# Kernel tuning notes

Hardware: AMD Instinct MI355X
Metric: run time of the kernel (lower is better)

The kernel has to match this reference:

```python
import jax, jax.numpy as jnp
import numpy as np
from jax import lax

B, C, L, K = 16, 128, 16000, 256
STRIDE = 4
ITERS = 10
DT, TAU = 0.01, 0.1
THR = 0.5


def setup_inputs() -> dict:
    key = jax.random.key(0)
    k1, k2 = jax.random.split(key)
    mini_batch = jax.random.normal(k1, (B, 1, L), dtype=jnp.float32)
    # dictionary / filterbank weights (stand-in for cm.compute_weights())
    weights = jax.random.normal(k2, (C, 1, K), dtype=jnp.float32) / np.sqrt(K).astype(np.float32)
    return {"mini_batch": mini_batch, "weights": weights}


def _conv1d(x, w, stride):
    # x: [B, Cin, L], w: [Cout, Cin, K] -> [B, Cout, S]  (torch F.conv1d, VALID)
    return lax.conv_general_dilated(
        x, w, window_strides=(stride,), padding="VALID",
        dimension_numbers=("NCH", "OIH", "NCH"))


def _conv_transpose1d(a, w, stride):
    # a: [B, C, S], w: [C, 1, K] -> [B, 1, (S-1)*stride + K]  (torch F.conv_transpose1d)
    k = w.shape[-1]
    w_t = jnp.flip(jnp.swapaxes(w, 0, 1), -1)  # [1, C, K]
    return lax.conv_general_dilated(
        a, w_t, window_strides=(1,), padding=[(k - 1, k - 1)],
        lhs_dilation=(stride,), dimension_numbers=("NCH", "OIH", "NCH"))


def _hard_shrink(u, thr):
    return jnp.where(jnp.abs(u) > thr, u, jnp.zeros((), u.dtype))


def reference(mini_batch, weights):
    # LCA fixed-point dynamics:
    #   u <- u + dt/tau * (W*x - u - W*(W^T a) + a),  a = HardShrink(u, thr)
    step_size = jnp.float32(DT / TAU)
    drive = _conv1d(mini_batch, weights, STRIDE)  # [B, C, S] precomputed driver
    u0 = jnp.zeros_like(drive)

    def step(u, _):
        a = _hard_shrink(u, THR)
        recon = _conv_transpose1d(a, weights, STRIDE)      # [B, 1, L]
        feedback = _conv1d(recon, weights, STRIDE)          # [B, C, S]
        u_new = u + step_size * (drive - u - feedback + a)
        return u_new, None

    u, _ = lax.scan(step, u0, None, length=ITERS)
    a = _hard_shrink(u, THR)  # spikegram / sparse code
    return a
```

## Files before the change

kernel.cpp:

```cpp
#include <hip/hip_runtime.h>
#include <math.h>

#define BB 16
#define CC 128
#define LL 16000
#define KK 256
#define SS 3937
#define MM 4000
#define THRS 0.5f
#define STEP 0.1f

template<int MODE>
__global__ __launch_bounds__(256, 2) void k_conv(
    const float* __restrict__ in0,
    const float* __restrict__ W,
    float* __restrict__ drive,
    float* __restrict__ u)
{
    __shared__ __align__(16) float sW[2][128 * 68];
    __shared__ __align__(16) float sX[768];
    __shared__ int sFlag;

    const int tid = threadIdx.x;
    const int tx = tid & 15;
    const int ty = tid >> 4;
    const int s0 = blockIdx.x * 128;
    const int b  = blockIdx.y;

    const int sc = tid >> 1;
    const int sg = (tid & 1) * 8;
    const float4* W4 = (const float4*)W;

    if (tid == 0) sFlag = 0;
    __syncthreads();

    bool nz = false;
    #pragma unroll
    for (int h = 0; h < 3; ++h) {
        int t = tid + 256 * h;
        int l = 4 * s0 + t;
        float v = (l < LL) ? in0[b * LL + l] : 0.f;
        sX[t] = v;
        nz |= (v != 0.f);
    }
    if (MODE != 0) { if (nz) atomicOr(&sFlag, 1); }
    __syncthreads();

    float acc[8][8];
    #pragma unroll
    for (int i = 0; i < 8; ++i)
        #pragma unroll
        for (int j = 0; j < 8; ++j) acc[i][j] = 0.f;

    const bool doit = (MODE == 0) || (sFlag != 0);

    if (doit) {
        {
            float4* dst = (float4*)sW[0];
            #pragma unroll
            for (int w = 0; w < 8; ++w)
                dst[sc * 17 + sg + w] = W4[sc * 64 + sg + w];
        }
        __syncthreads();

        for (int kc = 0; kc < 4; ++kc) {
            float4 pre[8];
            if (kc < 3) {
                #pragma unroll
                for (int w = 0; w < 8; ++w)
                    pre[w] = W4[sc * 64 + (kc + 1) * 16 + sg + w];
            }

            const float* wbuf = sW[kc & 1];
            const int xoff = 64 * kc;

            for (int kk4 = 0; kk4 < 16; ++kk4) {
                float4 xq[8];
                #pragma unroll
                for (int j = 0; j < 8; ++j)
                    xq[j] = *(const float4*)&sX[4 * (tx + 16 * j) + xoff + 4 * kk4];
                float4 w4[8];
                #pragma unroll
                for (int i = 0; i < 8; ++i)
                    w4[i] = *(const float4*)&wbuf[(ty + 16 * i) * 68 + 4 * kk4];
                #pragma unroll
                for (int dk = 0; dk < 4; ++dk) {
                    #pragma unroll
                    for (int i = 0; i < 8; ++i) {
                        float wv = (&w4[i].x)[dk];
                        #pragma unroll
                        for (int j = 0; j < 8; ++j)
                            acc[i][j] = fmaf(wv, (&xq[j].x)[dk], acc[i][j]);
                    }
                }
            }

            if (kc < 3) {
                float4* dst = (float4*)sW[(kc + 1) & 1];
                #pragma unroll
                for (int w = 0; w < 8; ++w)
                    dst[sc * 17 + sg + w] = pre[w];
            }
            __syncthreads();
        }
    }

    #pragma unroll
    for (int j = 0; j < 8; ++j) {
        int s = s0 + tx + 16 * j;
        if (s < SS) {
            #pragma unroll
            for (int i = 0; i < 8; ++i) {
                int c = ty + 16 * i;
                size_t idx = (size_t)(b * CC + c) * SS + s;
                if (MODE == 0) {
                    float d = acc[i][j];
                    drive[idx] = d;
                    u[idx] = __fmul_rn(STEP, d);
                } else {
                    float uo = u[idx];
                    float dr = drive[idx];
                    float a  = (fabsf(uo) > THRS) ? uo : 0.f;
                    float t1 = __fsub_rn(dr, uo);
                    float t2 = __fsub_rn(t1, acc[i][j]);
                    float t3 = __fadd_rn(t2, a);
                    float t4 = __fmul_rn(STEP, t3);
                    float un = __fadd_rn(uo, t4);
                    if (MODE == 1) u[idx] = un;
                    else           u[idx] = (fabsf(un) > THRS) ? un : 0.f;
                }
            }
        }
    }
}

#define FMAC_DPP(ACC, WREG, AREG, QI) \
    asm("v_fmac_f32_dpp %0, %1, %2 row_newbcast:" #QI " row_mask:0xf bank_mask:0xf" \
        : "+v"(ACC) : "v"(WREG), "v"(AREG))

#define QSTEP2(WQ, QB, QI) { \
    float a_ = arow[16 * (QB) + (QI)]; \
    FMAC_DPP(accA, WQ.x, a_, QI); \
    FMAC_DPP(accB, WQ.y, a_, QI); }

#define QBLOCK2(WQ, QB) \
    QSTEP2(WQ, QB, 0)  QSTEP2(WQ, QB, 1)  QSTEP2(WQ, QB, 2)  QSTEP2(WQ, QB, 3)  \
    QSTEP2(WQ, QB, 4)  QSTEP2(WQ, QB, 5)  QSTEP2(WQ, QB, 6)  QSTEP2(WQ, QB, 7)  \
    QSTEP2(WQ, QB, 8)  QSTEP2(WQ, QB, 9)  QSTEP2(WQ, QB, 10) QSTEP2(WQ, QB, 11) \
    QSTEP2(WQ, QB, 12) QSTEP2(WQ, QB, 13) QSTEP2(WQ, QB, 14) QSTEP2(WQ, QB, 15)

__global__ __launch_bounds__(512, 1) void k_recon(
    const float* __restrict__ u,
    const float* __restrict__ W,
    float* __restrict__ recon)
{
    __shared__ __align__(16) float sA[32 * 320];
    __shared__ int sFlag;

    const int tid  = threadIdx.x;
    const int p    = tid & 15;
    const int ml   = tid & 255;
    const int rp   = (tid >> 8) << 1;
    const int m0 = blockIdx.x * 256;
    const int b  = blockIdx.y;
    const int m  = m0 + ml;

    if (tid == 0) sFlag = 0;
    __syncthreads();

    float accA = 0.f, accB = 0.f;

    const float* Wq0 = W + 4 * (63 - p)      + rp;
    const float* Wq1 = W + 4 * (63 - 16 - p) + rp;
    const float* Wq2 = W + 4 * (63 - 32 - p) + rp;
    const float* Wq3 = W + 4 * (63 - 48 - p) + rp;

    for (int cs = 0; cs < 4; ++cs) {
        const int c0 = cs * 32;

        bool nz = false;
        #pragma unroll
        for (int h = 0; h < 20; ++h) {
            int idx = tid + 512 * h;
            int cl  = idx / 320;
            int col = idx - cl * 320;
            int mm  = m0 - 63 + col;
            float v = 0.f;
            if (col < 319 && mm >= 0 && mm < SS) {
                float uu = u[(size_t)(b * CC + c0 + cl) * SS + mm];
                v = (fabsf(uu) > THRS) ? uu : 0.f;
            }
            sA[idx] = v;
            nz |= (v != 0.f);
        }
        if (nz) atomicOr(&sFlag, 1);

        __syncthreads();
        const int f = sFlag;
        __syncthreads();
        if (tid == 0) sFlag = 0;

        if (f) {
            float2 w0 = *(const float2*)(Wq0 + (size_t)c0 * KK);
            float2 w1 = *(const float2*)(Wq1 + (size_t)c0 * KK);
            float2 w2 = *(const float2*)(Wq2 + (size_t)c0 * KK);
            float2 w3 = *(const float2*)(Wq3 + (size_t)c0 * KK);

            for (int cl = 0; cl < 32; ++cl) {
                float2 n0, n1, n2, n3;
                if (cl < 31) {
                    size_t co = (size_t)(c0 + cl + 1) * KK;
                    n0 = *(const float2*)(Wq0 + co);
                    n1 = *(const float2*)(Wq1 + co);
                    n2 = *(const float2*)(Wq2 + co);
                    n3 = *(const float2*)(Wq3 + co);
                }

                const float* arow = sA + cl * 320 + ml;
                QBLOCK2(w0, 0)
                QBLOCK2(w1, 1)
                QBLOCK2(w2, 2)
                QBLOCK2(w3, 3)

                w0 = n0; w1 = n1; w2 = n2; w3 = n3;
            }
        }
        __syncthreads();
    }

    if (m < MM) {
        float2* o = (float2*)(recon + (size_t)b * LL + 4 * m + rp);
        *o = make_float2(accA, accB);
    }
}

extern "C" void kernel_launch(void* const* d_in, const int* in_sizes, int n_in,
                              void* d_out, int out_size, void* d_ws, size_t ws_size,
                              hipStream_t stream) {
    const float* x = (const float*)d_in[0];
    const float* W = (const float*)d_in[1];
    float* u = (float*)d_out;

    float* ws    = (float*)d_ws;
    float* drive = ws;
    float* recon = drive + (size_t)BB * CC * SS;

    dim3 gConv(31, 16);
    k_conv<0><<<gConv, 256, 0, stream>>>(x, W, drive, u);

    for (int it = 0; it < 9; ++it) {
        k_recon<<<dim3(16, 16), 512, 0, stream>>>(u, W, recon);
        if (it < 8)
            k_conv<1><<<gConv, 256, 0, stream>>>(recon, W, drive, u);
        else
            k_conv<2><<<gConv, 256, 0, stream>>>(recon, W, drive, u);
    }
}
```

Baseline: 1.817 ms.

## Double-buffer activation tiles in recon kernel to overlap loads with compute

The recon kernel now keeps two shared-memory buffers for the thresholded activations. It prefetches the next 32-channel chunk from global memory into registers while the current chunk is being computed, then writes it into the other buffer. Per-chunk nonzero flags become bits of one shared word, which removes one barrier per chunk. The cost is more LDS (two 40KB buffers) and 20 extra registers per thread, which could hurt occupancy in a kernel that already runs at one block per CU.

```diff
diff --git a/kernel.cpp b/kernel.cpp
--- a/kernel.cpp
+++ b/kernel.cpp
@@ -154,7 +154,7 @@
     const float* __restrict__ W,
     float* __restrict__ recon)
 {
-    __shared__ __align__(16) float sA[32 * 320];
+    __shared__ __align__(16) float sA[2][32 * 320];
     __shared__ int sFlag;
 
     const int tid  = threadIdx.x;
@@ -175,9 +175,7 @@
     const float* Wq2 = W + 4 * (63 - 32 - p) + rp;
     const float* Wq3 = W + 4 * (63 - 48 - p) + rp;
 
-    for (int cs = 0; cs < 4; ++cs) {
-        const int c0 = cs * 32;
-
+    {
         bool nz = false;
         #pragma unroll
         for (int h = 0; h < 20; ++h) {
@@ -187,36 +185,56 @@
             int mm  = m0 - 63 + col;
             float v = 0.f;
             if (col < 319 && mm >= 0 && mm < SS) {
-                float uu = u[(size_t)(b * CC + c0 + cl) * SS + mm];
+                float uu = u[(size_t)(b * CC + cl) * SS + mm];
                 v = (fabsf(uu) > THRS) ? uu : 0.f;
             }
-            sA[idx] = v;
+            sA[0][idx] = v;
             nz |= (v != 0.f);
         }
         if (nz) atomicOr(&sFlag, 1);
+    }
+
+    for (int cs = 0; cs < 4; ++cs) {
+        const int c0 = cs * 32;
 
         __syncthreads();
-        const int f = sFlag;
-        __syncthreads();
-        if (tid == 0) sFlag = 0;
+        const int f = (sFlag >> cs) & 1;
+
+        float pv[20];
+        if (cs < 3) {
+            const int c0n = (cs + 1) * 32;
+            #pragma unroll
+            for (int h = 0; h < 20; ++h) {
+                int idx = tid + 512 * h;
+                int cl  = idx / 320;
+                int col = idx - cl * 320;
+                int mm  = m0 - 63 + col;
+                float v = 0.f;
+                if (col < 319 && mm >= 0 && mm < SS)
+                    v = u[(size_t)(b * CC + c0n + cl) * SS + mm];
+                pv[h] = v;
+            }
+        }
 
         if (f) {
-            float2 w0 = *(const float2*)(Wq0 + (size_t)c0 * KK);
-            float2 w1 = *(const float2*)(Wq1 + (size_t)c0 * KK);
-            float2 w2 = *(const float2*)(Wq2 + (size_t)c0 * KK);
-            float2 w3 = *(const float2*)(Wq3 + (size_t)c0 * KK);
+            const float* buf = sA[cs & 1];
+            size_t co = (size_t)c0 * KK;
+            float2 w0 = *(const float2*)(Wq0 + co);
+            float2 w1 = *(const float2*)(Wq1 + co);
+            float2 w2 = *(const float2*)(Wq2 + co);
+            float2 w3 = *(const float2*)(Wq3 + co);
 
             for (int cl = 0; cl < 32; ++cl) {
                 float2 n0, n1, n2, n3;
                 if (cl < 31) {
-                    size_t co = (size_t)(c0 + cl + 1) * KK;
-                    n0 = *(const float2*)(Wq0 + co);
-                    n1 = *(const float2*)(Wq1 + co);
-                    n2 = *(const float2*)(Wq2 + co);
-                    n3 = *(const float2*)(Wq3 + co);
+                    size_t cn = (size_t)(c0 + cl + 1) * KK;
+                    n0 = *(const float2*)(Wq0 + cn);
+                    n1 = *(const float2*)(Wq1 + cn);
+                    n2 = *(const float2*)(Wq2 + cn);
+                    n3 = *(const float2*)(Wq3 + cn);
                 }
 
-                const float* arow = sA + cl * 320 + ml;
+                const float* arow = buf + cl * 320 + ml;
                 QBLOCK2(w0, 0)
                 QBLOCK2(w1, 1)
                 QBLOCK2(w2, 2)
@@ -225,7 +243,20 @@
                 w0 = n0; w1 = n1; w2 = n2; w3 = n3;
             }
         }
-        __syncthreads();
+
+        if (cs < 3) {
+            bool nz = false;
+            float* dst = sA[(cs + 1) & 1];
+            #pragma unroll
+            for (int h = 0; h < 20; ++h) {
+                int idx = tid + 512 * h;
+                float uu = pv[h];
+                float v = (fabsf(uu) > THRS) ? uu : 0.f;
+                dst[idx] = v;
+                nz |= (v != 0.f);
+            }
+            if (nz) atomicOr(&sFlag, 1 << (cs + 1));
+        }
     }
 
     if (m < MM) {
```

Result: faster. 1.703 ms, median of 2 (-6.3%).
